# Kernel optimization log

Measured on AMD Instinct MI355X. Metric: run time of the kernel, lower is better.

## Reference

```python
import jax, jax.numpy as jnp
import numpy as np
import math

B, SQ, SK, H, NH = 8, 512, 512, 768, 12
DH = H // NH

def setup_inputs() -> dict:
    key = jax.random.key(0)
    ks = jax.random.split(key, 8)
    s = 1.0 / math.sqrt(H)
    return {
        "hidden_states": jax.random.normal(ks[0], (B, SQ, H), jnp.float32),
        "context": jax.random.normal(ks[1], (B, SK, H), jnp.float32),
        "attention_mask": jax.random.randint(ks[2], (B, SK), 0, 2, jnp.int32),
        "Wq": jax.random.normal(ks[3], (H, H), jnp.float32) * s,
        "bq": jnp.zeros((H,), jnp.float32),
        "Wk": jax.random.normal(ks[4], (H, H), jnp.float32) * s,
        "bk": jnp.zeros((H,), jnp.float32),
        "Wv": jax.random.normal(ks[5], (H, H), jnp.float32) * s,
        "bv": jnp.zeros((H,), jnp.float32),
        "abs_pos_emb": jax.random.normal(ks[6], (512, DH), jnp.float32),
    }

def _heads(x):
    # [B, S, H] -> [B, NH, S, DH]
    b, s, _ = x.shape
    return x.reshape(b, s, NH, DH).transpose(0, 2, 1, 3)

def reference(hidden_states, context, attention_mask, Wq, bq, Wk, bk, Wv, bv, abs_pos_emb):
    q = _heads(hidden_states @ Wq.T + bq)   # [B,NH,SQ,DH]
    k = _heads(context @ Wk.T + bk)         # [B,NH,SK,DH]
    v = _heads(context @ Wv.T + bv)         # [B,NH,SK,DH]
    scores = jnp.einsum('bhqd,bhkd->bhqk', q, k)
    pos_k = abs_pos_emb[:context.shape[1]]          # [SK, DH]
    pos_q = abs_pos_emb[:hidden_states.shape[1]]    # [SQ, DH]
    pos_scores = jnp.einsum('bhqd,kd->bhqk', q + pos_q[None, None], pos_k)
    scores = (scores + pos_scores) / jnp.sqrt(jnp.float32(DH))
    mask_bias = jnp.where(attention_mask[:, None, None, :] == 0,
                          -jnp.inf, 0.0).astype(scores.dtype)
    scores = scores + mask_bias
    probs = jax.nn.softmax(scores, axis=-1)  # dropout is identity in eval
    out = jnp.einsum('bhqk,bhkd->bhqd', probs, v)
    b, _, sq, _ = out.shape
    return out.transpose(0, 2, 1, 3).reshape(b, sq, NH * DH)
```

## Files before the change

### kernel.cpp

```cpp
#include <hip/hip_runtime.h>
#include <hip/hip_bf16.h>
#include <stdint.h>

#define B_   8
#define SQ_  512
#define SK_  512
#define H_   768
#define NH_  12
#define DH_  64
#define BH_  (B_*NH_)
#define M_   (B_*SQ_)
#define NTOT (3*H_)

typedef __attribute__((ext_vector_type(8))) short short8;
typedef __attribute__((ext_vector_type(4))) float floatx4;
typedef __attribute__((ext_vector_type(4))) unsigned int uint4v;
typedef __attribute__((ext_vector_type(4))) unsigned short ushort4v;

#define MFMA16(a, b, c) __builtin_amdgcn_mfma_f32_16x16x32_bf16((a), (b), (c), 0, 0, 0)

__device__ __forceinline__ unsigned short f2b(float f) {
  union { __hip_bfloat16 h; unsigned short u; } c;
  c.h = __float2bfloat16(f);
  return c.u;
}
__device__ __forceinline__ float b2f(unsigned short u) {
  union { float f; unsigned u; } c; c.u = ((unsigned)u) << 16;
  return c.f;
}
__device__ __forceinline__ short8 ld8(const unsigned short* p) {
  union { uint4v u; short8 s; } c;
  c.u = *(const uint4v*)p;
  return c.s;
}
__device__ __forceinline__ unsigned cvt2(float a, float b) {
  union { __hip_bfloat162 h; unsigned u; } c;
  c.h = __float22bfloat162_rn(float2{a, b});
  return c.u;
}
__device__ __forceinline__ ushort4v cvt4(floatx4 v) {
  union { unsigned u[2]; ushort4v s; } c;
  c.u[0] = cvt2(v.x, v.y);
  c.u[1] = cvt2(v.z, v.w);
  return c.s;
}

#define SEG_X   (M_*H_)
#define SEG_XC  (2*SEG_X)
#define SEG_W1  (H_*H_)
#define SEG_WE  (SEG_XC + 3*SEG_W1)
#define SEG_BE  (SEG_WE + NTOT)
#define SEG_PE  (SEG_BE + SQ_*DH_)

__global__ __launch_bounds__(256) void pack_kernel(
    const float* __restrict__ hid, const float* __restrict__ ctx,
    const float* __restrict__ Wq, const float* __restrict__ Wk, const float* __restrict__ Wv,
    const float* __restrict__ bq, const float* __restrict__ bk, const float* __restrict__ bv,
    const float* __restrict__ pos,
    unsigned short* __restrict__ Xh, unsigned short* __restrict__ Xc,
    unsigned short* __restrict__ Wa, float* __restrict__ Ba,
    unsigned short* __restrict__ Pb)
{
  int i = (blockIdx.x * 256 + threadIdx.x) * 4;
  if (i < SEG_X) {
    floatx4 v = *(const floatx4*)(hid + i);
    *(ushort4v*)(Xh + i) = cvt4(v);
  } else if (i < SEG_XC) {
    int j = i - SEG_X;
    floatx4 v = *(const floatx4*)(ctx + j);
    *(ushort4v*)(Xc + j) = cvt4(v);
  } else if (i < SEG_WE) {
    int j = i - SEG_XC;
    const float* src; int o;
    if (j < SEG_W1)        { src = Wq; o = j; }
    else if (j < 2*SEG_W1) { src = Wk; o = j - SEG_W1; }
    else                   { src = Wv; o = j - 2*SEG_W1; }
    floatx4 v = *(const floatx4*)(src + o);
    *(ushort4v*)(Wa + j) = cvt4(v);
  } else if (i < SEG_BE) {
    int j = i - SEG_WE;
    #pragma unroll
    for (int t = 0; t < 4; ++t) {
      int jj = j + t;
      float v = (jj < H_) ? bq[jj] : (jj < 2*H_) ? bk[jj - H_] : bv[jj - 2*H_];
      Ba[jj] = v;
    }
  } else if (i < SEG_PE) {
    int j = i - SEG_BE;
    floatx4 v = *(const floatx4*)(pos + j);
    *(ushort4v*)(Pb + j) = cvt4(v);
  }
}

__global__ __launch_bounds__(256) void qkv_gemm(
    const unsigned short* __restrict__ Xh, const unsigned short* __restrict__ Xc,
    const unsigned short* __restrict__ W,  const float* __restrict__ bias,
    const unsigned short* __restrict__ Pb,
    unsigned short* __restrict__ qw, unsigned short* __restrict__ kw,
    unsigned short* __restrict__ vt, float* __restrict__ P2)
{
  __shared__ unsigned short As[128][72];
  __shared__ unsigned short Bs[128][72];

  int bx = blockIdx.x;
  int tid = threadIdx.x;
  int lane = tid & 63, wave = tid >> 6;
  int lc16 = lane & 15, quad = lane >> 4, kk = quad * 8;

  if (bx >= 576) {
    int pb = bx - 576;
    int q0 = (pb >> 2) * 128, k0 = (pb & 3) * 128;
    int wq = (wave & 1) * 64, wk = (wave >> 1) * 64;
    short8 aqf[4][2], akf[4][2];
    #pragma unroll
    for (int i = 0; i < 4; ++i) {
      const unsigned short* qr = Pb + (q0 + wq + i * 16 + lc16) * DH_;
      const unsigned short* kr = Pb + (k0 + wk + i * 16 + lc16) * DH_;
      aqf[i][0] = ld8(qr + kk);      aqf[i][1] = ld8(qr + 32 + kk);
      akf[i][0] = ld8(kr + kk);      akf[i][1] = ld8(kr + 32 + kk);
    }
    #pragma unroll
    for (int i = 0; i < 4; ++i) {
      #pragma unroll
      for (int jt = 0; jt < 4; ++jt) {
        floatx4 acc2 = (floatx4){0.f, 0.f, 0.f, 0.f};
        acc2 = MFMA16(aqf[i][0], akf[jt][0], acc2);
        acc2 = MFMA16(aqf[i][1], akf[jt][1], acc2);
        #pragma unroll
        for (int r = 0; r < 4; ++r)
          P2[(size_t)(q0 + wq + i * 16 + quad * 4 + r) * SK_ + (k0 + wk + jt * 16 + lc16)] = acc2[r];
      }
    }
    return;
  }

  int xcd = bx & 7, j = bx >> 3;
  int bm = (xcd >> 1) * 8 + j / 9;
  int bn = (xcd & 1) * 9 + j % 9;
  const unsigned short* X = (bn < 6) ? Xh : Xc;
  bool isV = (bn >= 12);
  int m0 = bm * 128, n0 = bn * 128;

  int wm = (wave & 1) * 64, wn = (wave >> 1) * 64;
  int srow = tid >> 3, sch = (tid & 7) * 8;

  unsigned short (*TA)[72] = isV ? As : Bs;
  unsigned short (*TB)[72] = isV ? Bs : As;
  int oa = isV ? wm : wn;
  int ob = isV ? wn : wm;

  floatx4 acc[4][4];
  #pragma unroll
  for (int i = 0; i < 4; ++i)
    #pragma unroll
    for (int jj = 0; jj < 4; ++jj) acc[i][jj] = (floatx4){0.f, 0.f, 0.f, 0.f};

  uint4v a[4], b[4];
  #pragma unroll
  for (int rp = 0; rp < 4; ++rp) {
    a[rp] = *(const uint4v*)&X[(m0 + srow + rp * 32) * H_ + sch];
    b[rp] = *(const uint4v*)&W[(n0 + srow + rp * 32) * H_ + sch];
  }

  for (int k0 = 0; k0 < H_; k0 += 64) {
    __syncthreads();
    #pragma unroll
    for (int rp = 0; rp < 4; ++rp) {
      *(uint4v*)&As[srow + rp * 32][sch] = a[rp];
      *(uint4v*)&Bs[srow + rp * 32][sch] = b[rp];
    }
    __syncthreads();

    if (k0 + 64 < H_) {
      #pragma unroll
      for (int rp = 0; rp < 4; ++rp) {
        a[rp] = *(const uint4v*)&X[(m0 + srow + rp * 32) * H_ + k0 + 64 + sch];
        b[rp] = *(const uint4v*)&W[(n0 + srow + rp * 32) * H_ + k0 + 64 + sch];
      }
    }

    #pragma unroll
    for (int s = 0; s < 2; ++s) {
      short8 af[4], bf[4];
      #pragma unroll
      for (int i = 0; i < 4; ++i) af[i] = ld8(&TA[oa + i * 16 + lc16][s * 32 + kk]);
      #pragma unroll
      for (int i = 0; i < 4; ++i) bf[i] = ld8(&TB[ob + i * 16 + lc16][s * 32 + kk]);
      #pragma unroll
      for (int mi = 0; mi < 4; ++mi)
        #pragma unroll
        for (int ni = 0; ni < 4; ++ni)
          acc[mi][ni] = MFMA16(af[mi], bf[ni], acc[mi][ni]);
    }
  }

  if (!isV) {
    #pragma unroll
    for (int mi = 0; mi < 4; ++mi) {
      #pragma unroll
      for (int ni = 0; ni < 4; ++ni) {
        int gn0 = n0 + wn + mi * 16 + quad * 4;
        int gs  = m0 + wm + ni * 16 + lc16;
        int bidx = gs >> 9, s0 = gs & 511;
        floatx4 bv4 = *(const floatx4*)&bias[gn0];
        if (gn0 < H_) {
          int h = gn0 >> 6, d0 = gn0 & 63;
          floatx4 v;
          #pragma unroll
          for (int r = 0; r < 4; ++r) v[r] = acc[mi][ni][r] + bv4[r];
          *(ushort4v*)(qw + (((bidx * NH_ + h) << 9) + s0) * DH_ + d0) = cvt4(v);
        } else {
          int g = gn0 - H_;
          int h = g >> 6, d0 = g & 63;
          ushort4v pk = *(const ushort4v*)(Pb + s0 * DH_ + d0);
          floatx4 v;
          #pragma unroll
          for (int r = 0; r < 4; ++r) v[r] = acc[mi][ni][r] + bv4[r] + b2f(pk[r]);
          *(ushort4v*)(kw + (((bidx * NH_ + h) << 9) + s0) * DH_ + d0) = cvt4(v);
        }
      }
    }
  } else {
    #pragma unroll
    for (int mi = 0; mi < 4; ++mi) {
      #pragma unroll
      for (int ni = 0; ni < 4; ++ni) {
        int gm0 = m0 + wm + mi * 16 + quad * 4;
        int gn  = n0 + wn + ni * 16 + lc16;
        float bvs = bias[gn];
        int bidx = gm0 >> 9, s0 = gm0 & 511;
        int g = gn - 2 * H_;
        int h = g >> 6, d = g & 63;
        floatx4 v;
        #pragma unroll
        for (int r = 0; r < 4; ++r) v[r] = acc[mi][ni][r] + bvs;
        *(ushort4v*)(vt + ((bidx * NH_ + h) * DH_ + d) * SK_ + s0) = cvt4(v);
      }
    }
  }
}

#define SCALE2 0.18033688011112042f
#define CPAD 136

__global__ __launch_bounds__(256) void attn_kernel(
    const unsigned short* __restrict__ qw, const unsigned short* __restrict__ kw,
    const unsigned short* __restrict__ vt, const float* __restrict__ P2,
    const int* __restrict__ mask, float* __restrict__ out)
{
  __shared__ unsigned short Sc[2][64][CPAD];
  __shared__ float mb2[SK_];
  __shared__ float red[64][4];

  int bx = blockIdx.x;
  int bh = bx % 96, qt = bx / 96;
  int b = bh / NH_, h = bh - b * NH_;
  int tid = threadIdx.x, lane = tid & 63, wave = tid >> 6;
  int lc16 = lane & 15, quad = lane >> 4, kk = quad * 8;

  for (int i = tid; i < SK_; i += 256)
    mb2[i] = mask[(b << 9) + i] ? 0.0f : -100000.0f;

  const unsigned short* qbase = qw + ((bh << 9) + qt * 64) * DH_;
  short8 aq[4][2];
  #pragma unroll
  for (int rt = 0; rt < 4; ++rt) {
    const unsigned short* qr = qbase + (rt * 16 + lc16) * DH_;
    aq[rt][0] = ld8(qr + kk);
    aq[rt][1] = ld8(qr + 32 + kk);
  }

  const unsigned short* kwb = kw + ((bh << 9)) * DH_;
  const unsigned short* vb0 = vt + (bh * DH_ + wave * 16 + lc16) * SK_;
  const float* p2b = P2 + (size_t)(qt * 64 + lc16) * SK_ + quad * 4;
  float rs[4] = {0.f, 0.f, 0.f, 0.f};
  floatx4 o[4];
  #pragma unroll
  for (int i = 0; i < 4; ++i) o[i] = (floatx4){0.f, 0.f, 0.f, 0.f};

  short8 cb0, cb1, nb0, nb1;
  floatx4 pc[4], pn[4];
  {
    int kcol = wave * 32;
    const unsigned short* kb = kwb + kcol * DH_;
    cb0 = ld8(kb + lc16 * DH_ + kk);
    cb1 = ld8(kb + lc16 * DH_ + 32 + kk);
    #pragma unroll
    for (int rt = 0; rt < 4; ++rt)
      pc[rt] = *(const floatx4*)(p2b + rt * 16 * SK_ + kcol);
  }

  __syncthreads();

  for (int chunk = 0; chunk < 4; ++chunk) {
    unsigned short (*S)[CPAD] = Sc[chunk & 1];

    short8 vf[4];
    #pragma unroll
    for (int ks = 0; ks < 4; ++ks) vf[ks] = ld8(vb0 + chunk * 128 + ks * 32 + kk);

    #pragma unroll
    for (int ct = 0; ct < 2; ++ct) {
      int s = chunk * 2 + ct;
      if (s < 7) {
        int kcol = ((s + 1) >> 1) * 128 + wave * 32 + ((s + 1) & 1) * 16;
        const unsigned short* kb = kwb + kcol * DH_;
        nb0 = ld8(kb + lc16 * DH_ + kk);
        nb1 = ld8(kb + lc16 * DH_ + 32 + kk);
        #pragma unroll
        for (int rt = 0; rt < 4; ++rt)
          pn[rt] = *(const floatx4*)(p2b + rt * 16 * SK_ + kcol);
      }
      int kcol = chunk * 128 + wave * 32 + ct * 16;
      floatx4 mk = *(const floatx4*)&mb2[kcol + quad * 4];
      floatx4 c[4];
      __builtin_amdgcn_s_setprio(1);
      #pragma unroll
      for (int rt = 0; rt < 4; ++rt) {
        c[rt] = pc[rt];
        c[rt] = MFMA16(cb0, aq[rt][0], c[rt]);
        c[rt] = MFMA16(cb1, aq[rt][1], c[rt]);
      }
      __builtin_amdgcn_s_setprio(0);
      int lcol = wave * 32 + ct * 16 + quad * 4;
      #pragma unroll
      for (int rt = 0; rt < 4; ++rt) {
        floatx4 ev;
        float sum = 0.f;
        #pragma unroll
        for (int r = 0; r < 4; ++r) {
          float e = __builtin_exp2f(c[rt][r] * SCALE2 + mk[r]);
          sum += e;
          ev[r] = e;
        }
        rs[rt] += sum;
        *(ushort4v*)&S[rt * 16 + lc16][lcol] = cvt4(ev);
      }
      cb0 = nb0; cb1 = nb1;
      #pragma unroll
      for (int rt = 0; rt < 4; ++rt) pc[rt] = pn[rt];
    }
    __syncthreads();

    __builtin_amdgcn_s_setprio(1);
    #pragma unroll
    for (int ks = 0; ks < 4; ++ks) {
      #pragma unroll
      for (int rt = 0; rt < 4; ++rt) {
        short8 pa = ld8(&S[rt * 16 + lc16][ks * 32 + kk]);
        o[rt] = MFMA16(pa, vf[ks], o[rt]);
      }
    }
    __builtin_amdgcn_s_setprio(0);
  }

  #pragma unroll
  for (int rt = 0; rt < 4; ++rt) {
    rs[rt] += __shfl_xor(rs[rt], 16, 64);
    rs[rt] += __shfl_xor(rs[rt], 32, 64);
  }
  if (quad == 0) {
    #pragma unroll
    for (int rt = 0; rt < 4; ++rt) red[rt * 16 + lc16][wave] = rs[rt];
  }
  __syncthreads();

  #pragma unroll
  for (int rt = 0; rt < 4; ++rt) {
    #pragma unroll
    for (int r = 0; r < 4; ++r) {
      int sl = rt * 16 + quad * 4 + r;
      float inv = 1.0f / (red[sl][0] + red[sl][1] + red[sl][2] + red[sl][3]);
      int s = qt * 64 + sl;
      out[((b << 9) + s) * H_ + h * DH_ + wave * 16 + lc16] = o[rt][r] * inv;
    }
  }
}

extern "C" void kernel_launch(void* const* d_in, const int* in_sizes, int n_in,
                              void* d_out, int out_size, void* d_ws, size_t ws_size,
                              hipStream_t stream) {
  (void)in_sizes; (void)n_in; (void)out_size; (void)ws_size;
  const float* hid  = (const float*)d_in[0];
  const float* ctx  = (const float*)d_in[1];
  const int*   mask = (const int*)d_in[2];
  const float* Wq   = (const float*)d_in[3];
  const float* bq   = (const float*)d_in[4];
  const float* Wk   = (const float*)d_in[5];
  const float* bk   = (const float*)d_in[6];
  const float* Wv   = (const float*)d_in[7];
  const float* bv   = (const float*)d_in[8];
  const float* pos  = (const float*)d_in[9];

  char* ws = (char*)d_ws;
  size_t off = 0;
  auto alloc = [&](size_t bytes) { char* p = ws + off; off = (off + bytes + 255) & ~(size_t)255; return p; };
  unsigned short* Xh = (unsigned short*)alloc((size_t)SEG_X * 2);
  unsigned short* Xc = (unsigned short*)alloc((size_t)SEG_X * 2);
  unsigned short* Wa = (unsigned short*)alloc((size_t)3 * SEG_W1 * 2);
  float*          Ba = (float*)alloc((size_t)NTOT * 4);
  unsigned short* qw = (unsigned short*)alloc((size_t)BH_ * SQ_ * DH_ * 2);
  unsigned short* kw = (unsigned short*)alloc((size_t)BH_ * SK_ * DH_ * 2);
  unsigned short* vt = (unsigned short*)alloc((size_t)BH_ * DH_ * SK_ * 2);
  unsigned short* Pb = (unsigned short*)alloc((size_t)SQ_ * DH_ * 2);
  float*          P2 = (float*)alloc((size_t)SQ_ * SK_ * 4);

  int pack_blocks = (SEG_PE / 4 + 255) / 256;
  pack_kernel<<<pack_blocks, 256, 0, stream>>>(hid, ctx, Wq, Wk, Wv, bq, bk, bv, pos, Xh, Xc, Wa, Ba, Pb);
  qkv_gemm<<<32 * 18 + 16, 256, 0, stream>>>(Xh, Xc, Wa, Ba, Pb, qw, kw, vt, P2);
  attn_kernel<<<BH_ * 8, 256, 0, stream>>>(qw, kw, vt, P2, mask, (float*)d_out);
}
```

Measured before the change: 155.4 us.

## Use direct global-to-LDS loads with double-buffered, XOR-swizzled tiles in QKV GEMM

The QKV projection GEMM now loads its A and B tiles straight from global memory into LDS with global_load_lds, instead of staging them through registers. The tiles are double-buffered, so the next K-slice is fetched while MFMAs run on the current one, and waits use explicit vmcnt counters plus raw barriers. The padded row layout is replaced by an XOR swizzle on 16-byte chunks to avoid LDS bank conflicts. This doubles LDS use per block, which can cut occupancy, and correctness now depends on the hand-written waitcnt and barrier placement.

```diff
diff --git a/kernel.cpp b/kernel.cpp
--- a/kernel.cpp
+++ b/kernel.cpp
@@ -43,6 +43,11 @@
   c.u[0] = cvt2(v.x, v.y);
   c.u[1] = cvt2(v.z, v.w);
   return c.s;
+}
+__device__ __forceinline__ void gl_lds16(const unsigned short* g, unsigned short* l) {
+  __builtin_amdgcn_global_load_lds(
+      (const __attribute__((address_space(1))) unsigned int*)g,
+      (__attribute__((address_space(3))) unsigned int*)l, 16, 0, 0);
 }
 
 #define SEG_X   (M_*H_)
@@ -99,8 +104,8 @@
     unsigned short* __restrict__ qw, unsigned short* __restrict__ kw,
     unsigned short* __restrict__ vt, float* __restrict__ P2)
 {
-  __shared__ unsigned short As[128][72];
-  __shared__ unsigned short Bs[128][72];
+  __shared__ unsigned short As[2][128][64];
+  __shared__ unsigned short Bs[2][128][64];
 
   int bx = blockIdx.x;
   int tid = threadIdx.x;
@@ -142,10 +147,11 @@
   int m0 = bm * 128, n0 = bn * 128;
 
   int wm = (wave & 1) * 64, wn = (wave >> 1) * 64;
-  int srow = tid >> 3, sch = (tid & 7) * 8;
-
-  unsigned short (*TA)[72] = isV ? As : Bs;
-  unsigned short (*TB)[72] = isV ? Bs : As;
+
+  int srow = lane >> 3;
+  int swz  = (lane & 7) ^ srow;
+  int rb   = wave * 32;
+
   int oa = isV ? wm : wn;
   int ob = isV ? wn : wm;
 
@@ -155,43 +161,54 @@
     #pragma unroll
     for (int jj = 0; jj < 4; ++jj) acc[i][jj] = (floatx4){0.f, 0.f, 0.f, 0.f};
 
-  uint4v a[4], b[4];
-  #pragma unroll
-  for (int rp = 0; rp < 4; ++rp) {
-    a[rp] = *(const uint4v*)&X[(m0 + srow + rp * 32) * H_ + sch];
-    b[rp] = *(const uint4v*)&W[(n0 + srow + rp * 32) * H_ + sch];
-  }
-
-  for (int k0 = 0; k0 < H_; k0 += 64) {
-    __syncthreads();
-    #pragma unroll
-    for (int rp = 0; rp < 4; ++rp) {
-      *(uint4v*)&As[srow + rp * 32][sch] = a[rp];
-      *(uint4v*)&Bs[srow + rp * 32][sch] = b[rp];
-    }
-    __syncthreads();
-
-    if (k0 + 64 < H_) {
-      #pragma unroll
-      for (int rp = 0; rp < 4; ++rp) {
-        a[rp] = *(const uint4v*)&X[(m0 + srow + rp * 32) * H_ + k0 + 64 + sch];
-        b[rp] = *(const uint4v*)&W[(n0 + srow + rp * 32) * H_ + k0 + 64 + sch];
-      }
-    }
+  #pragma unroll
+  for (int c = 0; c < 4; ++c) {
+    int r = rb + c * 8;
+    gl_lds16(&X[(m0 + r + srow) * H_ + swz * 8], &As[0][r][0]);
+    gl_lds16(&W[(n0 + r + srow) * H_ + swz * 8], &Bs[0][r][0]);
+  }
+
+  for (int t = 0; t < 12; ++t) {
+    int cur = t & 1;
+    if (t < 11) {
+      int k0n = (t + 1) * 64;
+      #pragma unroll
+      for (int c = 0; c < 4; ++c) {
+        int r = rb + c * 8;
+        gl_lds16(&X[(m0 + r + srow) * H_ + k0n + swz * 8], &As[cur ^ 1][r][0]);
+        gl_lds16(&W[(n0 + r + srow) * H_ + k0n + swz * 8], &Bs[cur ^ 1][r][0]);
+      }
+      asm volatile("s_waitcnt vmcnt(8)" ::: "memory");
+    } else {
+      asm volatile("s_waitcnt vmcnt(0)" ::: "memory");
+    }
+    __builtin_amdgcn_sched_barrier(0);
+    __builtin_amdgcn_s_barrier();
+    __builtin_amdgcn_sched_barrier(0);
+
+    unsigned short (*Acur)[64] = As[cur];
+    unsigned short (*Bcur)[64] = Bs[cur];
+    unsigned short (*TA)[64] = isV ? Acur : Bcur;
+    unsigned short (*TB)[64] = isV ? Bcur : Acur;
 
     #pragma unroll
     for (int s = 0; s < 2; ++s) {
       short8 af[4], bf[4];
-      #pragma unroll
-      for (int i = 0; i < 4; ++i) af[i] = ld8(&TA[oa + i * 16 + lc16][s * 32 + kk]);
-      #pragma unroll
-      for (int i = 0; i < 4; ++i) bf[i] = ld8(&TB[ob + i * 16 + lc16][s * 32 + kk]);
+      int key = lc16 & 7;
+      int cswz = ((s * 4 + quad) ^ key) * 8;
+      #pragma unroll
+      for (int i = 0; i < 4; ++i) af[i] = ld8(&TA[oa + i * 16 + lc16][cswz]);
+      #pragma unroll
+      for (int i = 0; i < 4; ++i) bf[i] = ld8(&TB[ob + i * 16 + lc16][cswz]);
       #pragma unroll
       for (int mi = 0; mi < 4; ++mi)
         #pragma unroll
         for (int ni = 0; ni < 4; ++ni)
           acc[mi][ni] = MFMA16(af[mi], bf[ni], acc[mi][ni]);
     }
+    __builtin_amdgcn_sched_barrier(0);
+    __builtin_amdgcn_s_barrier();
+    __builtin_amdgcn_sched_barrier(0);
   }
 
   if (!isV) {
```

Result: slower. 161.7 us (+4.1%).

## Load QKV GEMM MFMA fragments directly from global memory, dropping LDS staging

Applied to the files above, without the earlier changes.

Removes the shared-memory tiles and barriers in the QKV projection GEMM. Each wave now reads its MFMA operand fragments straight from global memory, double-buffered across the two 32-wide k halves. This cuts LDS traffic and __syncthreads overhead. In exchange, the global loads are strided (16-byte chunks spread over rows) and each block re-reads data its waves used to share, so it leans on L2 cache hit rate.

```diff
diff --git a/kernel.cpp b/kernel.cpp
--- a/kernel.cpp
+++ b/kernel.cpp
@@ -99,9 +99,6 @@
     unsigned short* __restrict__ qw, unsigned short* __restrict__ kw,
     unsigned short* __restrict__ vt, float* __restrict__ P2)
 {
-  __shared__ unsigned short As[128][72];
-  __shared__ unsigned short Bs[128][72];
-
   int bx = blockIdx.x;
   int tid = threadIdx.x;
   int lane = tid & 63, wave = tid >> 6;
@@ -142,12 +139,19 @@
   int m0 = bm * 128, n0 = bn * 128;
 
   int wm = (wave & 1) * 64, wn = (wave >> 1) * 64;
-  int srow = tid >> 3, sch = (tid & 7) * 8;
-
-  unsigned short (*TA)[72] = isV ? As : Bs;
-  unsigned short (*TB)[72] = isV ? Bs : As;
-  int oa = isV ? wm : wn;
-  int ob = isV ? wn : wm;
+
+  const unsigned short* Aop = isV ? X : W;
+  const unsigned short* Bop = isV ? W : X;
+  int ar0 = isV ? (m0 + wm) : (n0 + wn);
+  int br0 = isV ? (n0 + wn) : (m0 + wm);
+
+  const unsigned short* pa[4];
+  const unsigned short* pb[4];
+  #pragma unroll
+  for (int i = 0; i < 4; ++i) {
+    pa[i] = Aop + (size_t)(ar0 + i * 16 + lc16) * H_ + kk;
+    pb[i] = Bop + (size_t)(br0 + i * 16 + lc16) * H_ + kk;
+  }
 
   floatx4 acc[4][4];
   #pragma unroll
@@ -155,43 +159,28 @@
     #pragma unroll
     for (int jj = 0; jj < 4; ++jj) acc[i][jj] = (floatx4){0.f, 0.f, 0.f, 0.f};
 
-  uint4v a[4], b[4];
-  #pragma unroll
-  for (int rp = 0; rp < 4; ++rp) {
-    a[rp] = *(const uint4v*)&X[(m0 + srow + rp * 32) * H_ + sch];
-    b[rp] = *(const uint4v*)&W[(n0 + srow + rp * 32) * H_ + sch];
-  }
-
-  for (int k0 = 0; k0 < H_; k0 += 64) {
-    __syncthreads();
-    #pragma unroll
-    for (int rp = 0; rp < 4; ++rp) {
-      *(uint4v*)&As[srow + rp * 32][sch] = a[rp];
-      *(uint4v*)&Bs[srow + rp * 32][sch] = b[rp];
-    }
-    __syncthreads();
-
-    if (k0 + 64 < H_) {
-      #pragma unroll
-      for (int rp = 0; rp < 4; ++rp) {
-        a[rp] = *(const uint4v*)&X[(m0 + srow + rp * 32) * H_ + k0 + 64 + sch];
-        b[rp] = *(const uint4v*)&W[(n0 + srow + rp * 32) * H_ + k0 + 64 + sch];
-      }
-    }
-
-    #pragma unroll
-    for (int s = 0; s < 2; ++s) {
-      short8 af[4], bf[4];
-      #pragma unroll
-      for (int i = 0; i < 4; ++i) af[i] = ld8(&TA[oa + i * 16 + lc16][s * 32 + kk]);
-      #pragma unroll
-      for (int i = 0; i < 4; ++i) bf[i] = ld8(&TB[ob + i * 16 + lc16][s * 32 + kk]);
-      #pragma unroll
-      for (int mi = 0; mi < 4; ++mi)
-        #pragma unroll
-        for (int ni = 0; ni < 4; ++ni)
-          acc[mi][ni] = MFMA16(af[mi], bf[ni], acc[mi][ni]);
-    }
+  short8 a0[4], b0[4], a1[4], b1[4];
+  #pragma unroll
+  for (int i = 0; i < 4; ++i) { a0[i] = ld8(pa[i]); b0[i] = ld8(pb[i]); }
+
+  for (int ks = 0; ks < 12; ++ks) {
+    int kc = ks * 64;
+    #pragma unroll
+    for (int i = 0; i < 4; ++i) { a1[i] = ld8(pa[i] + kc + 32); b1[i] = ld8(pb[i] + kc + 32); }
+    #pragma unroll
+    for (int mi = 0; mi < 4; ++mi)
+      #pragma unroll
+      for (int ni = 0; ni < 4; ++ni)
+        acc[mi][ni] = MFMA16(a0[mi], b0[ni], acc[mi][ni]);
+    if (ks < 11) {
+      #pragma unroll
+      for (int i = 0; i < 4; ++i) { a0[i] = ld8(pa[i] + kc + 64); b0[i] = ld8(pb[i] + kc + 64); }
+    }
+    #pragma unroll
+    for (int mi = 0; mi < 4; ++mi)
+      #pragma unroll
+      for (int ni = 0; ni < 4; ++ni)
+        acc[mi][ni] = MFMA16(a1[mi], b1[ni], acc[mi][ni]);
   }
 
   if (!isV) {
```

Measured after the change: 201.4 us. +29.6%, slower.
